# Kernel optimization log

Measured on AMD Instinct MI355X. Metric: run time of the kernel, lower is better.

Reference implementation:

```python
import jax, jax.numpy as jnp
import numpy as np

DIM = 1024
HID = 4096          # dim * hidden_mult
E = 8               # num_experts (E-1 routed + 1 shared)
TOPK = 2
ALPHA = 2.0
B, T = 1, 2048
DOWN_SCALE = 0.01


def setup_inputs() -> dict:
    key = jax.random.key(0)
    ks = jax.random.split(key, 8)
    s = 1.0 / np.sqrt(DIM)   # torch Linear default init bound (kaiming-uniform-ish)
    sh = 1.0 / np.sqrt(HID)
    return {
        "x": jax.random.normal(ks[0], (B, T, DIM), jnp.float32),
        "w_router": jax.random.uniform(ks[1], (DIM, E), jnp.float32, -s, s),
        # routed experts stacked on leading axis [E-1, ...]
        "w_up": jax.random.uniform(ks[2], (E - 1, DIM, HID), jnp.float32, -s, s),
        "w_gate": jax.random.uniform(ks[3], (E - 1, DIM, HID), jnp.float32, -s, s),
        "w_down": jax.random.normal(ks[4], (E - 1, HID, DIM), jnp.float32) * DOWN_SCALE,
        # shared expert
        "ws_up": jax.random.uniform(ks[5], (DIM, HID), jnp.float32, -s, s),
        "ws_gate": jax.random.uniform(ks[6], (DIM, HID), jnp.float32, -s, s),
        "ws_down": jax.random.normal(ks[7], (HID, DIM), jnp.float32) * DOWN_SCALE,
    }


def reference(x, w_router, w_up, w_gate, w_down, ws_up, ws_gate, ws_down):
    # router: softmax in fp32, cast back (matches torch code)
    logits = x @ w_router                                        # [b,t,E]
    probs = jax.nn.softmax(logits.astype(jnp.float32), axis=-1).astype(logits.dtype)
    topk_vals, topk_idx = jax.lax.top_k(probs, TOPK)             # [b,t,TOPK]

    # all routed experts' SwiGLU on every token (faithful to the dense-masked original)
    up = jnp.einsum('btd,edh->ebth', x, w_up)                    # [E-1,b,t,H]
    gate = jax.nn.silu(jnp.einsum('btd,edh->ebth', x, w_gate))
    exp_out = jnp.einsum('ebth,ehd->ebtd', up * gate, w_down)    # [E-1,b,t,d]

    out = jnp.zeros_like(x)
    eids = jnp.arange(E - 1)
    # NOTE: original loops i in range(top_k - 1) -> only top-1 routed expert used
    for i in range(TOPK - 1):
        idx_i = topk_idx[..., i]                                 # [b,t]
        sel = (idx_i[None, :, :] == eids[:, None, None]).astype(x.dtype)  # [E-1,b,t]
        gathered = jnp.einsum('ebt,ebtd->btd', sel, exp_out)
        out = out + ALPHA * topk_vals[..., i:i + 1] * gathered

    shared = ((x @ ws_up) * jax.nn.silu(x @ ws_gate)) @ ws_down
    return out + shared
```

## Files before the change

kernel.cpp:

```cpp
#include <hip/hip_runtime.h>
#include <hip/hip_fp16.h>

#define TNUM 2048
#define DIMS 1024
#define HIDS 4096
#define NEXP 8
#define NROUT 7
#define ALPHAF 2.0f

typedef __attribute__((ext_vector_type(4))) float floatx4;
typedef _Float16 half8 __attribute__((ext_vector_type(8)));
typedef unsigned short ushort_t;

static __device__ __forceinline__ ushort_t f2h(float f) {
    return __half_as_ushort(__float2half(f));
}

static __device__ __forceinline__ void async16(ushort_t* lds, const ushort_t* g) {
#if __has_builtin(__builtin_amdgcn_global_load_lds)
    __builtin_amdgcn_global_load_lds(
        (const __attribute__((address_space(1))) unsigned int*)g,
        (__attribute__((address_space(3))) unsigned int*)lds, 16, 0, 0);
#else
    int l = threadIdx.x & 63;
    *(uint4*)(lds + l * 8) = *(const uint4*)g;
#endif
}

__global__ __launch_bounds__(256) void router_kernel(
    const float* __restrict__ x, const float* __restrict__ wr,
    int* __restrict__ idx, float* __restrict__ wtok)
{
    int tok = blockIdx.x * 4 + (threadIdx.x >> 6);
    int lane = threadIdx.x & 63;
    const float* xp = x + (size_t)tok * DIMS;
    float acc[NEXP];
#pragma unroll
    for (int e = 0; e < NEXP; ++e) acc[e] = 0.f;
    for (int d = lane; d < DIMS; d += 64) {
        float xv = xp[d];
        const float* wrow = wr + d * NEXP;
#pragma unroll
        for (int e = 0; e < NEXP; ++e) acc[e] += xv * wrow[e];
    }
#pragma unroll
    for (int off = 32; off > 0; off >>= 1) {
#pragma unroll
        for (int e = 0; e < NEXP; ++e) acc[e] += __shfl_xor(acc[e], off, 64);
    }
    if (lane == 0) {
        float mx = acc[0];
#pragma unroll
        for (int e = 1; e < NEXP; ++e) mx = fmaxf(mx, acc[e]);
        float s = 0.f, pe[NEXP];
#pragma unroll
        for (int e = 0; e < NEXP; ++e) { pe[e] = __expf(acc[e] - mx); s += pe[e]; }
        int best = 0; float bv = acc[0];
#pragma unroll
        for (int e = 1; e < NEXP; ++e) if (acc[e] > bv) { bv = acc[e]; best = e; }
        if (best == NROUT) { idx[tok] = 0; wtok[tok] = 0.f; }
        else               { idx[tok] = best; wtok[tok] = ALPHAF * pe[best] / s; }
    }
}

__global__ void zero_counts_kernel(int* counts) {
    if (threadIdx.x < NROUT) counts[threadIdx.x] = 0;
}

__global__ __launch_bounds__(256) void build_lists_kernel(
    const int* __restrict__ idx, int* __restrict__ counts, int* __restrict__ lists)
{
    int t = blockIdx.x * 256 + threadIdx.x;
    int e = idx[t];
    int pos = atomicAdd(&counts[e], 1);
    lists[e * TNUM + pos] = t;
}

__global__ __launch_bounds__(256) void x2h_kernel(
    const float* __restrict__ x, ushort_t* __restrict__ x16)
{
    int i = (blockIdx.x * 256 + threadIdx.x) * 4;
    float4 v = *(const float4*)(x + i);
    ushort_t tmp[4] = { f2h(v.x), f2h(v.y), f2h(v.z), f2h(v.w) };
    *(uint2*)(x16 + i) = *(const uint2*)tmp;
}

__global__ __launch_bounds__(256) void repack_kernel(
    const float* __restrict__ wu, const float* __restrict__ wg, const float* __restrict__ wd,
    const float* __restrict__ su, const float* __restrict__ sg, const float* __restrict__ sd,
    ushort_t* __restrict__ wugT, ushort_t* __restrict__ wdT)
{
    int g = blockIdx.x;
    const float* src; ushort_t* dst; int N, K, gateAdd; bool ug;
    int nt, kt;
    if (g < 16384) {
        int slice = g >> 10, r = g & 1023;
        nt = r >> 4; kt = r & 15;
        K = DIMS; N = HIDS; ug = true;
        if (slice < 7)        { src = wu + (size_t)slice * DIMS * HIDS;       dst = wugT + (size_t)slice * 2 * HIDS * DIMS; gateAdd = 0; }
        else if (slice < 14)  { src = wg + (size_t)(slice - 7) * DIMS * HIDS; dst = wugT + (size_t)(slice - 7) * 2 * HIDS * DIMS; gateAdd = 32; }
        else if (slice == 14) { src = su; dst = wugT + (size_t)7 * 2 * HIDS * DIMS; gateAdd = 0; }
        else                  { src = sg; dst = wugT + (size_t)7 * 2 * HIDS * DIMS; gateAdd = 32; }
    } else {
        int gd = g - 16384; int slice = gd >> 10, r = gd & 1023;
        nt = r & 15; kt = r >> 4;
        K = HIDS; N = DIMS; ug = false; gateAdd = 0;
        if (slice < 7) { src = wd + (size_t)slice * HIDS * DIMS; dst = wdT + (size_t)slice * DIMS * HIDS; }
        else           { src = sd;                               dst = wdT + (size_t)7 * DIMS * HIDS; }
    }
    int n0 = nt * 64, k0 = kt * 64;

    __shared__ ushort_t T[64 * 66];
    int t = threadIdx.x;
    int kr = t >> 2, nc = (t & 3) * 16;
    const float* sp = src + (size_t)(k0 + kr) * N + n0 + nc;
    float v[16];
    *(float4*)&v[0]  = *(const float4*)sp;
    *(float4*)&v[4]  = *(const float4*)(sp + 4);
    *(float4*)&v[8]  = *(const float4*)(sp + 8);
    *(float4*)&v[12] = *(const float4*)(sp + 12);
#pragma unroll
    for (int j = 0; j < 16; ++j) T[(nc + j) * 66 + kr] = f2h(v[j]);
    __syncthreads();

    int rn = t >> 2, kc = (t & 3) * 16;
    ushort_t ov[16];
#pragma unroll
    for (int j = 0; j < 8; ++j)
        *(unsigned int*)&ov[2 * j] = *(const unsigned int*)&T[rn * 66 + kc + 2 * j];
    int n = n0 + rn;
    size_t R = ug ? (size_t)(((n >> 5) << 6) + (n & 31) + gateAdd) : (size_t)n;
    ushort_t* dp = dst + R * K + k0 + kc;
    *(uint4*)dp       = *(const uint4*)&ov[0];
    *(uint4*)(dp + 8) = *(const uint4*)&ov[8];
}

__global__ __launch_bounds__(256) void upgate_gemm(
    const ushort_t* __restrict__ x16, const ushort_t* __restrict__ wugT,
    ushort_t* __restrict__ hcat,
    const int* __restrict__ lists, const int* __restrict__ counts,
    const float* __restrict__ wtok)
{
    int e = blockIdx.z;
    bool routed = e < NROUT;
    int cnt = routed ? counts[e] : TNUM;
    int m0 = blockIdx.y * 128;
    if (m0 >= cnt) return;
    int n0 = blockIdx.x * 128;
    const ushort_t* B = wugT + (size_t)e * 2 * HIDS * DIMS;

    __shared__ ushort_t As[128 * 64];
    __shared__ ushort_t Bs[128 * 64];
    __shared__ int rowTok[128];
    int t = threadIdx.x;
    if (t < 128) {
        int i = m0 + t;
        rowTok[t] = (i < cnt) ? (routed ? lists[e * TNUM + i] : i) : -1;
    }
    __syncthreads();

    int w = t >> 6, l = t & 63;
    const ushort_t *gA[4], *gB[4]; ushort_t *lA[4], *lB[4];
#pragma unroll
    for (int p = 0; p < 4; ++p) {
        int slot = p * 256 + t, row = slot >> 3, ch = (slot & 7) ^ (row & 7);
        int tok = rowTok[row]; if (tok < 0) tok = 0;
        gA[p] = x16 + (size_t)tok * DIMS + ch * 8;
        gB[p] = B + (size_t)(n0 + row) * DIMS + ch * 8;
        lA[p] = &As[(p * 256 + w * 64) * 8];
        lB[p] = &Bs[(p * 256 + w * 64) * 8];
    }

    floatx4 acc[4][4];
#pragma unroll
    for (int i = 0; i < 4; ++i)
#pragma unroll
        for (int j = 0; j < 4; ++j) acc[i][j] = (floatx4){0.f, 0.f, 0.f, 0.f};

    int wr = (w >> 1) * 64, wc = (w & 1) * 64;
    int fr = l & 15, fq = l >> 4;

    for (int k0 = 0; k0 < DIMS; k0 += 64) {
#pragma unroll
        for (int p = 0; p < 4; ++p) {
            async16(lA[p], gA[p]); gA[p] += 64;
            async16(lB[p], gB[p]); gB[p] += 64;
        }
        __syncthreads();
#pragma unroll
        for (int kk = 0; kk < 2; ++kk) {
            int gc = kk * 4 + fq;
            half8 a[4], b[4];
#pragma unroll
            for (int i = 0; i < 4; ++i) {
                int r = wr + i * 16 + fr;
                a[i] = *(const half8*)&As[r * 64 + ((gc ^ (r & 7)) << 3)];
            }
#pragma unroll
            for (int j = 0; j < 4; ++j) {
                int r = wc + j * 16 + fr;
                b[j] = *(const half8*)&Bs[r * 64 + ((gc ^ (r & 7)) << 3)];
            }
#pragma unroll
            for (int i = 0; i < 4; ++i)
#pragma unroll
                for (int j = 0; j < 4; ++j)
                    acc[i][j] = __builtin_amdgcn_mfma_f32_16x16x32_f16(a[i], b[j], acc[i][j], 0, 0, 0);
        }
        __syncthreads();
    }

    int cq = l & 15, rq = (l >> 4) * 4;
    int nbase = (n0 + wc) >> 1;
    size_t hoff = routed ? HIDS : 0;
#pragma unroll
    for (int i = 0; i < 4; ++i) {
#pragma unroll
        for (int r = 0; r < 4; ++r) {
            int m = wr + i * 16 + rq + r;
            int tok = rowTok[m];
            if (tok < 0) continue;
            float sc = routed ? wtok[tok] : 1.f;
            ushort_t* hp = hcat + (size_t)tok * (2 * HIDS) + hoff + nbase;
#pragma unroll
            for (int j = 0; j < 2; ++j) {
                float u = acc[i][j][r], gg = acc[i][j + 2][r];
                float h = sc * u * (gg / (1.f + __expf(-gg)));
                hp[j * 16 + cq] = f2h(h);
            }
        }
    }
}

__global__ __launch_bounds__(256) void down_gemm(
    const ushort_t* __restrict__ hcat, const ushort_t* __restrict__ wdT,
    float* __restrict__ out,
    const int* __restrict__ lists, const int* __restrict__ counts)
{
    int e = blockIdx.z;
    int cnt = counts[e];
    int m0 = blockIdx.y * 128;
    if (m0 >= cnt) return;
    int n0 = blockIdx.x * 64;
    const ushort_t* BS = wdT + (size_t)NROUT * DIMS * HIDS;
    const ushort_t* BE = wdT + (size_t)e * DIMS * HIDS;

    __shared__ ushort_t As[128 * 64];
    __shared__ ushort_t Bs[64 * 64];
    __shared__ int rowTok[128];
    int t = threadIdx.x;
    if (t < 128) {
        int i = m0 + t;
        rowTok[t] = (i < cnt) ? lists[e * TNUM + i] : -1;
    }
    __syncthreads();

    int w = t >> 6, l = t & 63;
    const ushort_t* gA[4]; ushort_t* lA[4];
    size_t bOff[2]; ushort_t* lB[2];
#pragma unroll
    for (int p = 0; p < 4; ++p) {
        int slot = p * 256 + t, row = slot >> 3, ch = (slot & 7) ^ (row & 7);
        int tok = rowTok[row]; if (tok < 0) tok = 0;
        gA[p] = hcat + (size_t)tok * (2 * HIDS) + ch * 8;
        lA[p] = &As[(p * 256 + w * 64) * 8];
    }
#pragma unroll
    for (int q = 0; q < 2; ++q) {
        int slot = q * 256 + t, row = slot >> 3, ch = (slot & 7) ^ (row & 7);
        bOff[q] = (size_t)(n0 + row) * HIDS + ch * 8;
        lB[q] = &Bs[(q * 256 + w * 64) * 8];
    }

    floatx4 acc[4][2];
#pragma unroll
    for (int i = 0; i < 4; ++i)
#pragma unroll
        for (int j = 0; j < 2; ++j) acc[i][j] = (floatx4){0.f, 0.f, 0.f, 0.f};

    int wr = (w >> 1) * 64, wc = (w & 1) * 32;
    int fr = l & 15, fq = l >> 4;

#pragma unroll 1
    for (int half = 0; half < 2; ++half) {
        const ushort_t* Bsrc = half ? BE : BS;
        for (int k0 = 0; k0 < HIDS; k0 += 64) {
#pragma unroll
            for (int p = 0; p < 4; ++p) { async16(lA[p], gA[p]); gA[p] += 64; }
#pragma unroll
            for (int q = 0; q < 2; ++q) { async16(lB[q], Bsrc + bOff[q] + k0); }
            __syncthreads();
#pragma unroll
            for (int kk = 0; kk < 2; ++kk) {
                int gc = kk * 4 + fq;
                half8 a[4], b[2];
#pragma unroll
                for (int i = 0; i < 4; ++i) {
                    int r = wr + i * 16 + fr;
                    a[i] = *(const half8*)&As[r * 64 + ((gc ^ (r & 7)) << 3)];
                }
#pragma unroll
                for (int j = 0; j < 2; ++j) {
                    int r = wc + j * 16 + fr;
                    b[j] = *(const half8*)&Bs[r * 64 + ((gc ^ (r & 7)) << 3)];
                }
#pragma unroll
                for (int i = 0; i < 4; ++i)
#pragma unroll
                    for (int j = 0; j < 2; ++j)
                        acc[i][j] = __builtin_amdgcn_mfma_f32_16x16x32_f16(a[i], b[j], acc[i][j], 0, 0, 0);
            }
            __syncthreads();
        }
    }

    int cq = l & 15, rq = (l >> 4) * 4;
#pragma unroll
    for (int i = 0; i < 4; ++i) {
#pragma unroll
        for (int r = 0; r < 4; ++r) {
            int m = wr + i * 16 + rq + r;
            int tok = rowTok[m];
            if (tok < 0) continue;
            float* op = out + (size_t)tok * DIMS + n0 + wc;
#pragma unroll
            for (int j = 0; j < 2; ++j) op[j * 16 + cq] = acc[i][j][r];
        }
    }
}

extern "C" void kernel_launch(void* const* d_in, const int* in_sizes, int n_in,
                              void* d_out, int out_size, void* d_ws, size_t ws_size,
                              hipStream_t stream)
{
    const float* x  = (const float*)d_in[0];
    const float* wr = (const float*)d_in[1];
    const float* wu = (const float*)d_in[2];
    const float* wg = (const float*)d_in[3];
    const float* wd = (const float*)d_in[4];
    const float* su = (const float*)d_in[5];
    const float* sg = (const float*)d_in[6];
    const float* sd = (const float*)d_in[7];
    float* out = (float*)d_out;

    char* ws = (char*)d_ws;
    size_t off = 0;
    ushort_t* wugT = (ushort_t*)(ws + off); off += (size_t)NEXP * 2 * HIDS * DIMS * 2;
    ushort_t* wdT  = (ushort_t*)(ws + off); off += (size_t)NEXP * DIMS * HIDS * 2;
    ushort_t* x16  = (ushort_t*)(ws + off); off += (size_t)TNUM * DIMS * 2;
    ushort_t* hcat = (ushort_t*)(ws + off); off += (size_t)TNUM * 2 * HIDS * 2;
    float* wtok    = (float*)(ws + off);    off += TNUM * 4;
    int* idx       = (int*)(ws + off);      off += TNUM * 4;
    int* counts    = (int*)(ws + off);      off += 64;
    int* lists     = (int*)(ws + off);      off += (size_t)NROUT * TNUM * 4;

    router_kernel<<<TNUM / 4, 256, 0, stream>>>(x, wr, idx, wtok);
    zero_counts_kernel<<<1, 64, 0, stream>>>(counts);
    build_lists_kernel<<<TNUM / 256, 256, 0, stream>>>(idx, counts, lists);
    x2h_kernel<<<TNUM * DIMS / 1024, 256, 0, stream>>>(x, x16);
    repack_kernel<<<24576, 256, 0, stream>>>(wu, wg, wd, su, sg, sd, wugT, wdT);

    upgate_gemm<<<dim3(2 * HIDS / 128, TNUM / 128, NEXP), 256, 0, stream>>>(
        x16, wugT, hcat, lists, counts, wtok);
    down_gemm<<<dim3(DIMS / 64, TNUM / 128, NROUT), 256, 0, stream>>>(
        hcat, wdT, out, lists, counts);
}
```

Before: 696.4 us.

## Split-K down GEMM into four partial slices with reduction; enlarge repack tiles

The down GEMM now splits its K dimension (shared and routed halves, each split in two) across four grid slices. Each slice uses a 128x128 output tile and writes fp32 partials, and a new reduce kernel sums them into the output. Separately, the weight repack kernel moves from 64x64 to 128x128 tiles with a padded LDS stride, cutting the block count. The aim is more parallelism and better per-tile MFMA reuse in the down projection, at the cost of 32MB of partial-sum traffic and an extra kernel launch.

```diff
diff --git a/kernel.cpp b/kernel.cpp
--- a/kernel.cpp
+++ b/kernel.cpp
@@ -85,6 +85,7 @@
     *(uint2*)(x16 + i) = *(const uint2*)tmp;
 }
 
+#define LDK 136
 __global__ __launch_bounds__(256) void repack_kernel(
     const float* __restrict__ wu, const float* __restrict__ wg, const float* __restrict__ wd,
     const float* __restrict__ su, const float* __restrict__ sg, const float* __restrict__ sd,
@@ -93,46 +94,43 @@
     int g = blockIdx.x;
     const float* src; ushort_t* dst; int N, K, gateAdd; bool ug;
     int nt, kt;
-    if (g < 16384) {
-        int slice = g >> 10, r = g & 1023;
-        nt = r >> 4; kt = r & 15;
+    if (g < 4096) {
+        int slice = g >> 8, r = g & 255;
+        nt = r >> 3; kt = r & 7;
         K = DIMS; N = HIDS; ug = true;
         if (slice < 7)        { src = wu + (size_t)slice * DIMS * HIDS;       dst = wugT + (size_t)slice * 2 * HIDS * DIMS; gateAdd = 0; }
         else if (slice < 14)  { src = wg + (size_t)(slice - 7) * DIMS * HIDS; dst = wugT + (size_t)(slice - 7) * 2 * HIDS * DIMS; gateAdd = 32; }
         else if (slice == 14) { src = su; dst = wugT + (size_t)7 * 2 * HIDS * DIMS; gateAdd = 0; }
         else                  { src = sg; dst = wugT + (size_t)7 * 2 * HIDS * DIMS; gateAdd = 32; }
     } else {
-        int gd = g - 16384; int slice = gd >> 10, r = gd & 1023;
-        nt = r & 15; kt = r >> 4;
+        int gd = g - 4096; int slice = gd >> 8, r = gd & 255;
+        nt = r & 7; kt = r >> 3;
         K = HIDS; N = DIMS; ug = false; gateAdd = 0;
         if (slice < 7) { src = wd + (size_t)slice * HIDS * DIMS; dst = wdT + (size_t)slice * DIMS * HIDS; }
         else           { src = sd;                               dst = wdT + (size_t)7 * DIMS * HIDS; }
     }
-    int n0 = nt * 64, k0 = kt * 64;
-
-    __shared__ ushort_t T[64 * 66];
+    int n0 = nt * 128, k0 = kt * 128;
+
+    __shared__ ushort_t T[128 * LDK];
     int t = threadIdx.x;
-    int kr = t >> 2, nc = (t & 3) * 16;
+    int kr = t >> 1, nc = (t & 1) * 64;
     const float* sp = src + (size_t)(k0 + kr) * N + n0 + nc;
-    float v[16];
-    *(float4*)&v[0]  = *(const float4*)sp;
-    *(float4*)&v[4]  = *(const float4*)(sp + 4);
-    *(float4*)&v[8]  = *(const float4*)(sp + 8);
-    *(float4*)&v[12] = *(const float4*)(sp + 12);
-#pragma unroll
-    for (int j = 0; j < 16; ++j) T[(nc + j) * 66 + kr] = f2h(v[j]);
+    float v[64];
+#pragma unroll
+    for (int q = 0; q < 16; ++q)
+        *(float4*)&v[q * 4] = *(const float4*)(sp + q * 4);
+#pragma unroll
+    for (int j = 0; j < 64; ++j)
+        T[(nc + j) * LDK + kr] = f2h(v[j]);
     __syncthreads();
 
-    int rn = t >> 2, kc = (t & 3) * 16;
-    ushort_t ov[16];
-#pragma unroll
-    for (int j = 0; j < 8; ++j)
-        *(unsigned int*)&ov[2 * j] = *(const unsigned int*)&T[rn * 66 + kc + 2 * j];
+    int rn = t >> 1, kc = (t & 1) * 64;
     int n = n0 + rn;
     size_t R = ug ? (size_t)(((n >> 5) << 6) + (n & 31) + gateAdd) : (size_t)n;
     ushort_t* dp = dst + R * K + k0 + kc;
-    *(uint4*)dp       = *(const uint4*)&ov[0];
-    *(uint4*)(dp + 8) = *(const uint4*)&ov[8];
+#pragma unroll
+    for (int q = 0; q < 8; ++q)
+        *(uint4*)(dp + q * 8) = *(const uint4*)&T[rn * LDK + kc + q * 8];
 }
 
 __global__ __launch_bounds__(256) void upgate_gemm(
@@ -234,19 +232,22 @@
 
 __global__ __launch_bounds__(256) void down_gemm(
     const ushort_t* __restrict__ hcat, const ushort_t* __restrict__ wdT,
-    float* __restrict__ out,
+    float* __restrict__ part,
     const int* __restrict__ lists, const int* __restrict__ counts)
 {
-    int e = blockIdx.z;
+    int z = blockIdx.z;
+    int e = z >> 2, s = z & 3;
     int cnt = counts[e];
     int m0 = blockIdx.y * 128;
     if (m0 >= cnt) return;
-    int n0 = blockIdx.x * 64;
-    const ushort_t* BS = wdT + (size_t)NROUT * DIMS * HIDS;
-    const ushort_t* BE = wdT + (size_t)e * DIMS * HIDS;
+    int n0 = blockIdx.x * 128;
+    const ushort_t* B = (s < 2)
+        ? wdT + (size_t)NROUT * DIMS * HIDS + (size_t)s * 2048
+        : wdT + (size_t)e * DIMS * HIDS + (size_t)(s - 2) * 2048;
+    size_t aoff = (size_t)s * 2048;
 
     __shared__ ushort_t As[128 * 64];
-    __shared__ ushort_t Bs[64 * 64];
+    __shared__ ushort_t Bs[128 * 64];
     __shared__ int rowTok[128];
     int t = threadIdx.x;
     if (t < 128) {
@@ -256,62 +257,54 @@
     __syncthreads();
 
     int w = t >> 6, l = t & 63;
-    const ushort_t* gA[4]; ushort_t* lA[4];
-    size_t bOff[2]; ushort_t* lB[2];
+    const ushort_t *gA[4], *gB[4]; ushort_t *lA[4], *lB[4];
 #pragma unroll
     for (int p = 0; p < 4; ++p) {
         int slot = p * 256 + t, row = slot >> 3, ch = (slot & 7) ^ (row & 7);
         int tok = rowTok[row]; if (tok < 0) tok = 0;
-        gA[p] = hcat + (size_t)tok * (2 * HIDS) + ch * 8;
+        gA[p] = hcat + (size_t)tok * (2 * HIDS) + aoff + ch * 8;
+        gB[p] = B + (size_t)(n0 + row) * HIDS + ch * 8;
         lA[p] = &As[(p * 256 + w * 64) * 8];
-    }
-#pragma unroll
-    for (int q = 0; q < 2; ++q) {
-        int slot = q * 256 + t, row = slot >> 3, ch = (slot & 7) ^ (row & 7);
-        bOff[q] = (size_t)(n0 + row) * HIDS + ch * 8;
-        lB[q] = &Bs[(q * 256 + w * 64) * 8];
-    }
-
-    floatx4 acc[4][2];
+        lB[p] = &Bs[(p * 256 + w * 64) * 8];
+    }
+
+    floatx4 acc[4][4];
 #pragma unroll
     for (int i = 0; i < 4; ++i)
 #pragma unroll
-        for (int j = 0; j < 2; ++j) acc[i][j] = (floatx4){0.f, 0.f, 0.f, 0.f};
-
-    int wr = (w >> 1) * 64, wc = (w & 1) * 32;
+        for (int j = 0; j < 4; ++j) acc[i][j] = (floatx4){0.f, 0.f, 0.f, 0.f};
+
+    int wr = (w >> 1) * 64, wc = (w & 1) * 64;
     int fr = l & 15, fq = l >> 4;
 
-#pragma unroll 1
-    for (int half = 0; half < 2; ++half) {
-        const ushort_t* Bsrc = half ? BE : BS;
-        for (int k0 = 0; k0 < HIDS; k0 += 64) {
-#pragma unroll
-            for (int p = 0; p < 4; ++p) { async16(lA[p], gA[p]); gA[p] += 64; }
-#pragma unroll
-            for (int q = 0; q < 2; ++q) { async16(lB[q], Bsrc + bOff[q] + k0); }
-            __syncthreads();
-#pragma unroll
-            for (int kk = 0; kk < 2; ++kk) {
-                int gc = kk * 4 + fq;
-                half8 a[4], b[2];
-#pragma unroll
-                for (int i = 0; i < 4; ++i) {
-                    int r = wr + i * 16 + fr;
-                    a[i] = *(const half8*)&As[r * 64 + ((gc ^ (r & 7)) << 3)];
-                }
-#pragma unroll
-                for (int j = 0; j < 2; ++j) {
-                    int r = wc + j * 16 + fr;
-                    b[j] = *(const half8*)&Bs[r * 64 + ((gc ^ (r & 7)) << 3)];
-                }
-#pragma unroll
-                for (int i = 0; i < 4; ++i)
-#pragma unroll
-                    for (int j = 0; j < 2; ++j)
-                        acc[i][j] = __builtin_amdgcn_mfma_f32_16x16x32_f16(a[i], b[j], acc[i][j], 0, 0, 0);
-            }
-            __syncthreads();
-        }
+    for (int k0 = 0; k0 < 2048; k0 += 64) {
+#pragma unroll
+        for (int p = 0; p < 4; ++p) {
+            async16(lA[p], gA[p]); gA[p] += 64;
+            async16(lB[p], gB[p]); gB[p] += 64;
+        }
+        __syncthreads();
+#pragma unroll
+        for (int kk = 0; kk < 2; ++kk) {
+            int gc = kk * 4 + fq;
+            half8 a[4], b[4];
+#pragma unroll
+            for (int i = 0; i < 4; ++i) {
+                int r = wr + i * 16 + fr;
+                a[i] = *(const half8*)&As[r * 64 + ((gc ^ (r & 7)) << 3)];
+            }
+#pragma unroll
+            for (int j = 0; j < 4; ++j) {
+                int r = wc + j * 16 + fr;
+                b[j] = *(const half8*)&Bs[r * 64 + ((gc ^ (r & 7)) << 3)];
+            }
+#pragma unroll
+            for (int i = 0; i < 4; ++i)
+#pragma unroll
+                for (int j = 0; j < 4; ++j)
+                    acc[i][j] = __builtin_amdgcn_mfma_f32_16x16x32_f16(a[i], b[j], acc[i][j], 0, 0, 0);
+        }
+        __syncthreads();
     }
 
     int cq = l & 15, rq = (l >> 4) * 4;
@@ -322,11 +315,24 @@
             int m = wr + i * 16 + rq + r;
             int tok = rowTok[m];
             if (tok < 0) continue;
-            float* op = out + (size_t)tok * DIMS + n0 + wc;
-#pragma unroll
-            for (int j = 0; j < 2; ++j) op[j * 16 + cq] = acc[i][j][r];
-        }
-    }
+            float* pp = part + ((size_t)s * TNUM + tok) * DIMS + n0 + wc;
+#pragma unroll
+            for (int j = 0; j < 4; ++j) pp[j * 16 + cq] = acc[i][j][r];
+        }
+    }
+}
+
+__global__ __launch_bounds__(256) void reduce_kernel(
+    const float* __restrict__ part, float* __restrict__ out)
+{
+    size_t i = ((size_t)blockIdx.x * 256 + threadIdx.x) * 4;
+    float4 a = *(const float4*)(part + i);
+    float4 b = *(const float4*)(part + (size_t)TNUM * DIMS + i);
+    float4 c = *(const float4*)(part + (size_t)2 * TNUM * DIMS + i);
+    float4 d = *(const float4*)(part + (size_t)3 * TNUM * DIMS + i);
+    float4 o = make_float4(a.x + b.x + c.x + d.x, a.y + b.y + c.y + d.y,
+                           a.z + b.z + c.z + d.z, a.w + b.w + c.w + d.w);
+    *(float4*)(out + i) = o;
 }
 
 extern "C" void kernel_launch(void* const* d_in, const int* in_sizes, int n_in,
@@ -349,6 +355,7 @@
     ushort_t* wdT  = (ushort_t*)(ws + off); off += (size_t)NEXP * DIMS * HIDS * 2;
     ushort_t* x16  = (ushort_t*)(ws + off); off += (size_t)TNUM * DIMS * 2;
     ushort_t* hcat = (ushort_t*)(ws + off); off += (size_t)TNUM * 2 * HIDS * 2;
+    float* part    = (float*)(ws + off);    off += (size_t)4 * TNUM * DIMS * 4;
     float* wtok    = (float*)(ws + off);    off += TNUM * 4;
     int* idx       = (int*)(ws + off);      off += TNUM * 4;
     int* counts    = (int*)(ws + off);      off += 64;
@@ -358,10 +365,11 @@
     zero_counts_kernel<<<1, 64, 0, stream>>>(counts);
     build_lists_kernel<<<TNUM / 256, 256, 0, stream>>>(idx, counts, lists);
     x2h_kernel<<<TNUM * DIMS / 1024, 256, 0, stream>>>(x, x16);
-    repack_kernel<<<24576, 256, 0, stream>>>(wu, wg, wd, su, sg, sd, wugT, wdT);
+    repack_kernel<<<6144, 256, 0, stream>>>(wu, wg, wd, su, sg, sd, wugT, wdT);
 
     upgate_gemm<<<dim3(2 * HIDS / 128, TNUM / 128, NEXP), 256, 0, stream>>>(
         x16, wugT, hcat, lists, counts, wtok);
-    down_gemm<<<dim3(DIMS / 64, TNUM / 128, NROUT), 256, 0, stream>>>(
-        hcat, wdT, out, lists, counts);
-}
+    down_gemm<<<dim3(DIMS / 128, TNUM / 128, NROUT * 4), 256, 0, stream>>>(
+        hcat, wdT, part, lists, counts);
+    reduce_kernel<<<TNUM * DIMS / 1024, 256, 0, stream>>>(part, out);
+}
```

Measured after the change: 628.9 us. 1.11x faster.
